# Kernel tuning notes

Measured on AMD Instinct MI355X. Metric: run time of the kernel, lower is better.

The kernel has to match this reference:

```python
import jax, jax.numpy as jnp
import numpy as np

B, N, H = 32, 1024, 128
EPS = 1e-5


def setup_inputs() -> dict:
    key = jax.random.key(0)
    ks = jax.random.split(key, 9)
    node_embeddings = jax.random.normal(ks[0], (B, N, H), dtype=jnp.float32)
    edge_relations = jax.random.normal(ks[1], (B, N, N, 3), dtype=jnp.float32)
    adjacency = jax.random.randint(ks[2], (N, N), 0, 2, dtype=jnp.int32)
    s_msg = 1.0 / np.sqrt(H + 3)
    s_upd = 1.0 / np.sqrt(2 * H)
    W_msg = jax.random.uniform(ks[3], (H, H + 3), jnp.float32, -s_msg, s_msg)
    b_msg = jax.random.uniform(ks[4], (H,), jnp.float32, -s_msg, s_msg)
    W_upd = jax.random.uniform(ks[5], (H, 2 * H), jnp.float32, -s_upd, s_upd)
    b_upd = jax.random.uniform(ks[6], (H,), jnp.float32, -s_upd, s_upd)
    gamma = jnp.ones((H,), jnp.float32)
    beta = jnp.zeros((H,), jnp.float32)
    return {"node_embeddings": node_embeddings, "edge_relations": edge_relations,
            "adjacency": adjacency, "W_msg": W_msg, "b_msg": b_msg,
            "W_upd": W_upd, "b_upd": b_upd, "gamma": gamma, "beta": beta}


def reference(node_embeddings, edge_relations, adjacency, W_msg, b_msg, W_upd, b_upd, gamma, beta):
    # node_embeddings: [B,N,H]; edge_relations: [B,N,N,3]; adjacency: [N,N]
    b_, n_, h_ = node_embeddings.shape
    mask = (adjacency > 0).astype(node_embeddings.dtype)  # mask[j,i]=1 if i is neighbor of j
    # Split msg_nn weight: Linear(cat(h_i, e_ij)) = h_i @ W_h^T + e_ij @ W_e^T + b
    W_h = W_msg[:, :h_]   # [H,H]
    W_e = W_msg[:, h_:]   # [H,3]
    h_part = jnp.einsum('bih,oh->bio', node_embeddings, W_h)       # [B,N,H]
    msg_h = jnp.einsum('ji,bio->bjo', mask, h_part)                # aggregate sender linear part
    e_agg = jnp.einsum('bijc,ji->bjc', edge_relations, mask)       # aggregate edge feats first (memory-bound)
    msg_e = jnp.einsum('bjc,oc->bjo', e_agg, W_e)
    deg = mask.sum(axis=1)                                         # [N] in-degree of j
    messages = msg_h + msg_e + deg[None, :, None] * b_msg          # bias added once per edge
    # Dropout(0.2) is identity in inference; BatchNorm uses batch stats (training-mode math).
    upd_in = jnp.concatenate([node_embeddings, messages], axis=-1)  # [B,N,2H]
    updated = jax.nn.relu(jnp.einsum('bjk,ok->bjo', upd_in, W_upd) + b_upd)
    flat = updated.reshape(-1, h_)
    mean = flat.mean(axis=0)
    var = flat.var(axis=0)  # biased, as BatchNorm1d
    normed = (flat - mean) * jax.lax.rsqrt(var + EPS) * gamma + beta
    return normed.reshape(b_, n_, h_) + node_embeddings
```

## Files before the change

### kernel.cpp

```cpp
#include <hip/hip_runtime.h>
#include <hip/hip_bf16.h>

typedef _Float16 f16;
typedef f16 f16x4 __attribute__((ext_vector_type(4)));
typedef f16 f16x8 __attribute__((ext_vector_type(8)));
typedef float f32x4 __attribute__((ext_vector_type(4)));

#define BB 32
#define NN 1024
#define HH 128
#define ROWS (BB*NN)
#define EPS 1e-5f

__device__ __forceinline__ f16 f2h(float x) { return (f16)x; }

__global__ __launch_bounds__(256) void prep_k(
    const float* __restrict__ node, const int* __restrict__ adj,
    const float* __restrict__ W_msg, const float* __restrict__ W_upd,
    f16* __restrict__ mask_h, float* __restrict__ maskT, float* __restrict__ deg,
    f16* __restrict__ upd_in, f16* __restrict__ Wh, f16* __restrict__ Wupd,
    float* __restrict__ We, float* __restrict__ e_agg, float* __restrict__ sums)
{
  const int blk = blockIdx.x, t = threadIdx.x;
  if (blk < 1024) {
    const int j = blk;
    float d = 0.f;
    for (int i = t; i < NN; i += 256) {
      const int a = (adj[j*NN + i] > 0) ? 1 : 0;
      mask_h[j*NN + i] = a ? (f16)1.0f : (f16)0.0f;
      d += (float)a;
    }
    __shared__ float sh[256];
    sh[t] = d;
    for (int s = 128; s > 0; s >>= 1) {
      __syncthreads();
      if (t < s) sh[t] += sh[t + s];
    }
    __syncthreads();
    if (t == 0) deg[j] = sh[0];
  } else if (blk < 2048) {
    const int bi = (blk - 1024) & 31, bj = (blk - 1024) >> 5;
    __shared__ float tile[32][33];
    const int lx = t & 31, ly0 = t >> 5;
    for (int ly = ly0; ly < 32; ly += 8)
      tile[ly][lx] = (adj[(bj*32 + ly)*NN + bi*32 + lx] > 0) ? 1.0f : 0.0f;
    __syncthreads();
    for (int ly = ly0; ly < 32; ly += 8)
      maskT[(long)(bi*32 + ly)*NN + bj*32 + lx] = tile[lx][ly];
  } else if (blk < 4096) {
    const int base = (blk - 2048) * 512 + t;
    #pragma unroll
    for (int rep = 0; rep < 2; rep++) {
      const int idx = base + rep * 256;
      const float4 v = ((const float4*)node)[idx];
      f16x4 hv; hv[0] = f2h(v.x); hv[1] = f2h(v.y); hv[2] = f2h(v.z); hv[3] = f2h(v.w);
      const int row = idx >> 5;
      const int col = (idx & 31) << 2;
      *(f16x4*)&upd_in[(long)row*256 + col] = hv;
    }
  } else if (blk == 4096) {
    for (int idx = t; idx < HH*HH; idx += 256) {
      const int o = idx >> 7, h = idx & 127;
      Wh[idx] = f2h(W_msg[o*131 + h]);
    }
    for (int idx = t; idx < HH*256; idx += 256) {
      const int o = idx >> 8, k = idx & 255;
      Wupd[idx] = f2h(W_upd[o*256 + k]);
    }
    for (int idx = t; idx < HH*3; idx += 256) {
      const int o = idx / 3, c = idx % 3;
      We[idx] = W_msg[o*131 + 128 + c];
    }
    if (t < 256) sums[t] = 0.f;
  } else {
    const int base = (blk - 4097) * 3072 + t;
    #pragma unroll
    for (int r = 0; r < 12; r++) e_agg[base + r*256] = 0.f;
  }
}

__global__ __launch_bounds__(384) void eagg_k(
    const float* __restrict__ E, const float* __restrict__ maskT,
    float* __restrict__ e_agg)
{
  const int jt = blockIdx.x << 7;
  const int ih = blockIdx.y << 9;
  const int b  = blockIdx.z;
  const int t  = threadIdx.x;
  const int jl = t / 3, c = t % 3;
  const int j  = jt + jl;
  const float* Ep = E + (long)b*3145728 + (long)ih*3072 + jt*3 + t;
  const float* Mp = maskT + (long)ih*NN + j;
  float acc = 0.f;
  for (int i0 = 0; i0 < 512; i0 += 8) {
    float ev[8], mv[8];
    #pragma unroll
    for (int u = 0; u < 8; u++) ev[u] = Ep[(long)(i0 + u)*3072];
    #pragma unroll
    for (int u = 0; u < 8; u++) mv[u] = Mp[(long)(i0 + u)*NN];
    #pragma unroll
    for (int u = 0; u < 8; u++) acc = fmaf(mv[u], ev[u], acc);
  }
  atomicAdd(&e_agg[((long)b*NN + j)*3 + c], acc);
}

template<int MODE>
__global__ __launch_bounds__(256) void gemm_bt_k(
    const f16* __restrict__ Ag, long aBatch, int lda,
    const f16* __restrict__ Bg, long bBatch, int ldb,
    int K, void* __restrict__ outp,
    const float* __restrict__ deg, const float* __restrict__ b_msg,
    const float* __restrict__ e_agg, const float* __restrict__ We,
    const float* __restrict__ b_upd)
{
  const int mt = blockIdx.x, nt = blockIdx.y, bb = blockIdx.z;
  const f16* Ab = Ag + (long)bb*aBatch + (long)mt*128*lda;
  const f16* Bb = Bg + (long)bb*bBatch + (long)nt*128*ldb;
  __shared__ f16 As[128*32];
  __shared__ f16 Bs[128*32];
  const int tid  = threadIdx.x;
  const int lane = tid & 63;
  const int wave = tid >> 6;
  const int wm = (wave & 1) << 6, wn = (wave >> 1) << 6;

  f32x4 acc[4][4];
  #pragma unroll
  for (int i = 0; i < 4; i++)
    #pragma unroll
    for (int j = 0; j < 4; j++)
      #pragma unroll
      for (int r = 0; r < 4; r++) acc[i][j][r] = 0.f;

  for (int k0 = 0; k0 < K; k0 += 32) {
    #pragma unroll
    for (int p = 0; p < 2; p++) {
      const int q = (p << 8) + tid;
      const int row = q >> 2, ks = (q & 3) << 3;
      *(uint4*)&As[(row << 5) + ks] = *(const uint4*)&Ab[(long)row*lda + k0 + ks];
      *(uint4*)&Bs[(row << 5) + ks] = *(const uint4*)&Bb[(long)row*ldb + k0 + ks];
    }
    __syncthreads();
    f16x8 af[4], bf[4];
    #pragma unroll
    for (int i = 0; i < 4; i++) {
      af[i] = *(const f16x8*)&As[((wm + (i << 4) + (lane & 15)) << 5) + ((lane >> 4) << 3)];
      bf[i] = *(const f16x8*)&Bs[((wn + (i << 4) + (lane & 15)) << 5) + ((lane >> 4) << 3)];
    }
    #pragma unroll
    for (int i = 0; i < 4; i++)
      #pragma unroll
      for (int j = 0; j < 4; j++)
        acc[i][j] = __builtin_amdgcn_mfma_f32_16x16x32_f16(af[i], bf[j], acc[i][j], 0, 0, 0);
    __syncthreads();
  }

  const int rb = (lane >> 4) << 2, cb = lane & 15;
  if (MODE == 0) {
    f16* out = (f16*)outp + (long)bb * (HH*NN);
    #pragma unroll
    for (int i = 0; i < 4; i++)
      #pragma unroll
      for (int r = 0; r < 4; r++) {
        const int gm = (mt << 7) + wm + (i << 4) + rb + r;
        #pragma unroll
        for (int j = 0; j < 4; j++) {
          const int gn = (nt << 7) + wn + (j << 4) + cb;
          out[(long)gm*NN + gn] = f2h(acc[i][j][r]);
        }
      }
  } else if (MODE == 1) {
    f16* out = (f16*)outp;
    #pragma unroll
    for (int i = 0; i < 4; i++)
      #pragma unroll
      for (int r = 0; r < 4; r++) {
        const int gm = (mt << 7) + wm + (i << 4) + rb + r;
        const float dg = deg[gm];
        const long eb = ((long)bb*NN + gm)*3;
        const float e0 = e_agg[eb], e1 = e_agg[eb+1], e2 = e_agg[eb+2];
        #pragma unroll
        for (int j = 0; j < 4; j++) {
          const int gn = wn + (j << 4) + cb;
          const float v = acc[i][j][r] + dg*b_msg[gn]
                        + e0*We[gn*3] + e1*We[gn*3+1] + e2*We[gn*3+2];
          out[((long)bb*NN + gm)*256 + 128 + gn] = f2h(v);
        }
      }
  } else {
    float* out = (float*)outp;
    #pragma unroll
    for (int i = 0; i < 4; i++)
      #pragma unroll
      for (int r = 0; r < 4; r++) {
        const int gm = (mt << 7) + wm + (i << 4) + rb + r;
        #pragma unroll
        for (int j = 0; j < 4; j++) {
          const int gn = wn + (j << 4) + cb;
          const float v = acc[i][j][r] + b_upd[gn];
          out[(long)gm*HH + gn] = fmaxf(v, 0.f);
        }
      }
  }
}

__global__ __launch_bounds__(256) void stats_k(const float* __restrict__ upd,
                                               float* __restrict__ sums)
{
  const int t = threadIdx.x, o = t & 127, half = t >> 7;
  const long base = (long)blockIdx.x * 128;
  float s = 0.f, q = 0.f;
  for (int r = half; r < 128; r += 2) {
    const float v = upd[(base + r)*HH + o];
    s += v; q += v*v;
  }
  __shared__ float shs[256], shq[256];
  shs[t] = s; shq[t] = q;
  __syncthreads();
  if (t < 128) {
    atomicAdd(&sums[t],       shs[t] + shs[t + 128]);
    atomicAdd(&sums[128 + t], shq[t] + shq[t + 128]);
  }
}

__global__ __launch_bounds__(256) void final_k(const float* __restrict__ upd,
    const float* __restrict__ node, const float* __restrict__ sums,
    const float* __restrict__ gamma, const float* __restrict__ beta,
    float* __restrict__ out)
{
  const long idx = (long)blockIdx.x*256 + threadIdx.x;
  const float4 u  = ((const float4*)upd)[idx];
  const float4 nd = ((const float4*)node)[idx];
  const int ob = (idx & 31) << 2;
  const float inv = 1.0f/32768.0f;
  float4 res;
  #pragma unroll
  for (int c = 0; c < 4; c++) {
    const float m  = sums[ob + c]*inv;
    const float va = sums[128 + ob + c]*inv - m*m;
    const float sc = rsqrtf(va + EPS)*gamma[ob + c];
    ((float*)&res)[c] = (((const float*)&u)[c] - m)*sc + beta[ob + c]
                      + ((const float*)&nd)[c];
  }
  ((float4*)out)[idx] = res;
}

extern "C" void kernel_launch(void* const* d_in, const int* in_sizes, int n_in,
                              void* d_out, int out_size, void* d_ws, size_t ws_size,
                              hipStream_t stream) {
  const float* node  = (const float*)d_in[0];
  const float* E     = (const float*)d_in[1];
  const int*   adj   = (const int*)  d_in[2];
  const float* W_msg = (const float*)d_in[3];
  const float* b_msg = (const float*)d_in[4];
  const float* W_upd = (const float*)d_in[5];
  const float* b_upd = (const float*)d_in[6];
  const float* gamma = (const float*)d_in[7];
  const float* beta  = (const float*)d_in[8];
  float* out = (float*)d_out;

  char* p = (char*)d_ws;
  auto alloc = [&](size_t n) { void* r = (void*)p; p += (n + 255) & ~(size_t)255; return r; };
  f16*   upd_in   = (f16*)  alloc((size_t)ROWS*256*2);
  f16*   h_part_T = (f16*)  alloc((size_t)BB*HH*NN*2);
  f16*   mask_h   = (f16*)  alloc((size_t)NN*NN*2);
  float* maskT    = (float*)alloc((size_t)NN*NN*4);
  float* updated  = (float*)alloc((size_t)ROWS*HH*4);
  float* e_agg    = (float*)alloc((size_t)BB*NN*3*4);
  f16*   Wh       = (f16*)  alloc((size_t)HH*HH*2);
  f16*   Wupd     = (f16*)  alloc((size_t)HH*256*2);
  float* We       = (float*)alloc((size_t)HH*3*4);
  float* deg      = (float*)alloc((size_t)NN*4);
  float* sums     = (float*)alloc((size_t)256*4);

  prep_k<<<4129, 256, 0, stream>>>(node, adj, W_msg, W_upd, mask_h, maskT, deg,
                                   upd_in, Wh, Wupd, We, e_agg, sums);

  gemm_bt_k<0><<<dim3(1, 8, BB), 256, 0, stream>>>(
      Wh, 0, HH, upd_in, (long)NN*256, 256, HH, h_part_T,
      nullptr, nullptr, nullptr, nullptr, nullptr);

  eagg_k<<<dim3(8, 2, BB), 384, 0, stream>>>(E, maskT, e_agg);

  gemm_bt_k<1><<<dim3(8, 1, BB), 256, 0, stream>>>(
      mask_h, 0, NN, h_part_T, (long)HH*NN, NN, NN, upd_in,
      deg, b_msg, e_agg, We, nullptr);

  gemm_bt_k<2><<<dim3(256, 1, 1), 256, 0, stream>>>(
      upd_in, 0, 256, Wupd, 0, 256, 256, updated,
      nullptr, nullptr, nullptr, nullptr, b_upd);

  stats_k<<<256, 256, 0, stream>>>(updated, sums);
  final_k<<<4096, 256, 0, stream>>>(updated, node, sums, gamma, beta, out);
}
```

Before: 705.2 us.

## Fuse prep, edge aggregation and GEMMs; fold BN stats into update GEMM epilogue

Restructures the pipeline into fewer kernels. The mask transpose and f16 mask buffers are removed, and the mask is built from adjacency on the fly inside the GEMM and the edge aggregation. The h_part GEMM and the edge aggregation now run in one launch as separate block groups, and the f16 conversion of node embeddings is fused into the GEMM loads. BatchNorm column sums are computed in the update GEMM epilogue, and the updated activations are stored as f16. This cuts launches, intermediate traffic and the separate stats pass, at the cost of somewhat lower precision in the stored activations and a less coalesced edge-feature read pattern.

```diff
diff --git a/kernel.cpp b/kernel.cpp
--- a/kernel.cpp
+++ b/kernel.cpp
@@ -14,130 +14,115 @@
 
 __device__ __forceinline__ f16 f2h(float x) { return (f16)x; }
 
-__global__ __launch_bounds__(256) void prep_k(
-    const float* __restrict__ node, const int* __restrict__ adj,
+__global__ __launch_bounds__(256) void prep0_k(
     const float* __restrict__ W_msg, const float* __restrict__ W_upd,
-    f16* __restrict__ mask_h, float* __restrict__ maskT, float* __restrict__ deg,
-    f16* __restrict__ upd_in, f16* __restrict__ Wh, f16* __restrict__ Wupd,
-    float* __restrict__ We, float* __restrict__ e_agg, float* __restrict__ sums)
+    f16* __restrict__ Wh, f16* __restrict__ Wupd, float* __restrict__ We,
+    float* __restrict__ e_agg, float* __restrict__ deg, float* __restrict__ sums)
 {
   const int blk = blockIdx.x, t = threadIdx.x;
-  if (blk < 1024) {
-    const int j = blk;
-    float d = 0.f;
-    for (int i = t; i < NN; i += 256) {
-      const int a = (adj[j*NN + i] > 0) ? 1 : 0;
-      mask_h[j*NN + i] = a ? (f16)1.0f : (f16)0.0f;
-      d += (float)a;
-    }
-    __shared__ float sh[256];
-    sh[t] = d;
-    for (int s = 128; s > 0; s >>= 1) {
-      __syncthreads();
-      if (t < s) sh[t] += sh[t + s];
-    }
-    __syncthreads();
-    if (t == 0) deg[j] = sh[0];
-  } else if (blk < 2048) {
-    const int bi = (blk - 1024) & 31, bj = (blk - 1024) >> 5;
-    __shared__ float tile[32][33];
-    const int lx = t & 31, ly0 = t >> 5;
-    for (int ly = ly0; ly < 32; ly += 8)
-      tile[ly][lx] = (adj[(bj*32 + ly)*NN + bi*32 + lx] > 0) ? 1.0f : 0.0f;
-    __syncthreads();
-    for (int ly = ly0; ly < 32; ly += 8)
-      maskT[(long)(bi*32 + ly)*NN + bj*32 + lx] = tile[lx][ly];
-  } else if (blk < 4096) {
-    const int base = (blk - 2048) * 512 + t;
-    #pragma unroll
-    for (int rep = 0; rep < 2; rep++) {
-      const int idx = base + rep * 256;
-      const float4 v = ((const float4*)node)[idx];
-      f16x4 hv; hv[0] = f2h(v.x); hv[1] = f2h(v.y); hv[2] = f2h(v.z); hv[3] = f2h(v.w);
-      const int row = idx >> 5;
-      const int col = (idx & 31) << 2;
-      *(f16x4*)&upd_in[(long)row*256 + col] = hv;
-    }
-  } else if (blk == 4096) {
+  if (blk == 0) {
     for (int idx = t; idx < HH*HH; idx += 256) {
       const int o = idx >> 7, h = idx & 127;
       Wh[idx] = f2h(W_msg[o*131 + h]);
     }
-    for (int idx = t; idx < HH*256; idx += 256) {
-      const int o = idx >> 8, k = idx & 255;
-      Wupd[idx] = f2h(W_upd[o*256 + k]);
-    }
-    for (int idx = t; idx < HH*3; idx += 256) {
-      const int o = idx / 3, c = idx % 3;
-      We[idx] = W_msg[o*131 + 128 + c];
-    }
+  } else if (blk == 1) {
+    for (int idx = t; idx < HH*256; idx += 256)
+      Wupd[idx] = f2h(W_upd[idx]);
+  } else if (blk == 2) {
+    for (int idx = t; idx < HH*3; idx += 256)
+      We[idx] = W_msg[(idx/3)*131 + 128 + (idx % 3)];
     if (t < 256) sums[t] = 0.f;
+    for (int idx = t; idx < NN; idx += 256) deg[idx] = 0.f;
   } else {
-    const int base = (blk - 4097) * 3072 + t;
-    #pragma unroll
-    for (int r = 0; r < 12; r++) e_agg[base + r*256] = 0.f;
-  }
-}
-
-__global__ __launch_bounds__(384) void eagg_k(
-    const float* __restrict__ E, const float* __restrict__ maskT,
-    float* __restrict__ e_agg)
-{
-  const int jt = blockIdx.x << 7;
-  const int ih = blockIdx.y << 9;
-  const int b  = blockIdx.z;
-  const int t  = threadIdx.x;
-  const int jl = t / 3, c = t % 3;
-  const int j  = jt + jl;
-  const float* Ep = E + (long)b*3145728 + (long)ih*3072 + jt*3 + t;
-  const float* Mp = maskT + (long)ih*NN + j;
-  float acc = 0.f;
-  for (int i0 = 0; i0 < 512; i0 += 8) {
-    float ev[8], mv[8];
-    #pragma unroll
-    for (int u = 0; u < 8; u++) ev[u] = Ep[(long)(i0 + u)*3072];
-    #pragma unroll
-    for (int u = 0; u < 8; u++) mv[u] = Mp[(long)(i0 + u)*NN];
-    #pragma unroll
-    for (int u = 0; u < 8; u++) acc = fmaf(mv[u], ev[u], acc);
-  }
-  atomicAdd(&e_agg[((long)b*NN + j)*3 + c], acc);
-}
-
-template<int MODE>
-__global__ __launch_bounds__(256) void gemm_bt_k(
-    const f16* __restrict__ Ag, long aBatch, int lda,
-    const f16* __restrict__ Bg, long bBatch, int ldb,
-    int K, void* __restrict__ outp,
-    const float* __restrict__ deg, const float* __restrict__ b_msg,
-    const float* __restrict__ e_agg, const float* __restrict__ We,
-    const float* __restrict__ b_upd)
-{
-  const int mt = blockIdx.x, nt = blockIdx.y, bb = blockIdx.z;
-  const f16* Ab = Ag + (long)bb*aBatch + (long)mt*128*lda;
-  const f16* Bb = Bg + (long)bb*bBatch + (long)nt*128*ldb;
+    const int base = (blk - 3) * 24576 + t;
+    #pragma unroll
+    for (int r = 0; r < 96; r++) e_agg[base + r*256] = 0.f;
+  }
+}
+
+__global__ __launch_bounds__(256) void phaseB_k(
+    const float* __restrict__ node, const float* __restrict__ E,
+    const int* __restrict__ adj, const f16* __restrict__ Wh,
+    f16* __restrict__ h_part_T, float* __restrict__ e_agg,
+    float* __restrict__ deg)
+{
   __shared__ f16 As[128*32];
   __shared__ f16 Bs[128*32];
-  const int tid  = threadIdx.x;
-  const int lane = tid & 63;
-  const int wave = tid >> 6;
+  const int tid = threadIdx.x;
+
+  if (blockIdx.x >= 256) {
+    const int e  = blockIdx.x - 256;
+    const int bb = e >> 5;
+    const int r5 = e & 31;
+    const int jt = r5 & 3;
+    const int ih = r5 >> 2;
+    const int j  = (jt << 8) + tid;
+    const int i0 = ih << 7;
+    const float* Ep = E + (long)bb*3145728 + (long)i0*3072 + (long)j*3;
+    const int*   Ap = adj + (long)j*NN + i0;
+    float a0 = 0.f, a1 = 0.f, a2 = 0.f, dc = 0.f;
+    for (int ii = 0; ii < 128; ii += 8) {
+      const int4 m0 = *(const int4*)(Ap + ii);
+      const int4 m1 = *(const int4*)(Ap + ii + 4);
+      float ev[8][3];
+      #pragma unroll
+      for (int v = 0; v < 8; v++) {
+        const float* q = Ep + (long)(ii + v)*3072;
+        ev[v][0] = q[0]; ev[v][1] = q[1]; ev[v][2] = q[2];
+      }
+      const int mm[8] = {m0.x, m0.y, m0.z, m0.w, m1.x, m1.y, m1.z, m1.w};
+      #pragma unroll
+      for (int v = 0; v < 8; v++) {
+        const float m = (mm[v] > 0) ? 1.f : 0.f;
+        a0 = fmaf(m, ev[v][0], a0);
+        a1 = fmaf(m, ev[v][1], a1);
+        a2 = fmaf(m, ev[v][2], a2);
+        dc += m;
+      }
+    }
+    const long eb = ((long)bb*NN + j)*3;
+    atomicAdd(&e_agg[eb],     a0);
+    atomicAdd(&e_agg[eb + 1], a1);
+    atomicAdd(&e_agg[eb + 2], a2);
+    if (bb == 0) atomicAdd(&deg[j], dc);
+    return;
+  }
+
+  const int g  = blockIdx.x;
+  const int nt = g & 7, bb = g >> 3;
+  const int nbase = nt << 7;
+  const int lane = tid & 63, wave = tid >> 6;
   const int wm = (wave & 1) << 6, wn = (wave >> 1) << 6;
 
-  f32x4 acc[4][4];
-  #pragma unroll
-  for (int i = 0; i < 4; i++)
+  f32x4 acc[2][4];
+  #pragma unroll
+  for (int i = 0; i < 2; i++)
     #pragma unroll
     for (int j = 0; j < 4; j++)
       #pragma unroll
       for (int r = 0; r < 4; r++) acc[i][j][r] = 0.f;
-
-  for (int k0 = 0; k0 < K; k0 += 32) {
+  f32x4 acc2[2][4];
+  #pragma unroll
+  for (int i = 0; i < 2; i++)
+    #pragma unroll
+    for (int j = 0; j < 4; j++)
+      #pragma unroll
+      for (int r = 0; r < 4; r++) acc2[i][j][r] = 0.f;
+
+  for (int k0 = 0; k0 < HH; k0 += 32) {
     #pragma unroll
     for (int p = 0; p < 2; p++) {
       const int q = (p << 8) + tid;
       const int row = q >> 2, ks = (q & 3) << 3;
-      *(uint4*)&As[(row << 5) + ks] = *(const uint4*)&Ab[(long)row*lda + k0 + ks];
-      *(uint4*)&Bs[(row << 5) + ks] = *(const uint4*)&Bb[(long)row*ldb + k0 + ks];
+      *(uint4*)&As[(row << 5) + ks] = *(const uint4*)&Wh[(long)row*HH + k0 + ks];
+    }
+    #pragma unroll
+    for (int p = 0; p < 4; p++) {
+      const int q = (p << 8) + tid;
+      const int row = q >> 3, kc = (q & 7) << 2;
+      const float4 v = *(const float4*)&node[(long)((bb << 10) + nbase + row)*HH + k0 + kc];
+      f16x4 hv; hv[0] = f2h(v.x); hv[1] = f2h(v.y); hv[2] = f2h(v.z); hv[3] = f2h(v.w);
+      *(f16x4*)&Bs[(row << 5) + kc] = hv;
     }
     __syncthreads();
     f16x8 af[4], bf[4];
@@ -147,6 +132,80 @@
       bf[i] = *(const f16x8*)&Bs[((wn + (i << 4) + (lane & 15)) << 5) + ((lane >> 4) << 3)];
     }
     #pragma unroll
+    for (int i = 0; i < 2; i++)
+      #pragma unroll
+      for (int j = 0; j < 4; j++) {
+        acc[i][j]  = __builtin_amdgcn_mfma_f32_16x16x32_f16(af[i],     bf[j], acc[i][j],  0, 0, 0);
+        acc2[i][j] = __builtin_amdgcn_mfma_f32_16x16x32_f16(af[i + 2], bf[j], acc2[i][j], 0, 0, 0);
+      }
+    __syncthreads();
+  }
+
+  f16* out = h_part_T + (long)bb * (HH*NN);
+  const int rb = (lane >> 4) << 2, cb = lane & 15;
+  #pragma unroll
+  for (int i = 0; i < 4; i++)
+    #pragma unroll
+    for (int r = 0; r < 4; r++) {
+      const int gm = wm + (i << 4) + rb + r;
+      #pragma unroll
+      for (int j = 0; j < 4; j++) {
+        const int gn = nbase + wn + (j << 4) + cb;
+        const float v = (i < 2) ? acc[i][j][r] : acc2[i - 2][j][r];
+        out[(long)gm*NN + gn] = f2h(v);
+      }
+    }
+}
+
+__global__ __launch_bounds__(256) void gemm1_k(
+    const int* __restrict__ adj, const f16* __restrict__ hp,
+    const float* __restrict__ deg, const float* __restrict__ b_msg,
+    const float* __restrict__ e_agg, const float* __restrict__ We,
+    f16* __restrict__ msgs)
+{
+  const int mt = blockIdx.x, bb = blockIdx.z;
+  const int jb = mt << 7;
+  __shared__ f16 As[128*32];
+  __shared__ f16 Bs[128*32];
+  const int tid = threadIdx.x, lane = tid & 63, wave = tid >> 6;
+  const int wm = (wave & 1) << 6, wn = (wave >> 1) << 6;
+
+  f32x4 acc[4][4];
+  #pragma unroll
+  for (int i = 0; i < 4; i++)
+    #pragma unroll
+    for (int j = 0; j < 4; j++)
+      #pragma unroll
+      for (int r = 0; r < 4; r++) acc[i][j][r] = 0.f;
+
+  for (int k0 = 0; k0 < NN; k0 += 32) {
+    #pragma unroll
+    for (int p = 0; p < 4; p++) {
+      const int q = (p << 8) + tid;
+      const int row = q >> 3, kc = (q & 7) << 2;
+      const int4 m = *(const int4*)&adj[(long)(jb + row)*NN + k0 + kc];
+      f16x4 hv;
+      hv[0] = (m.x > 0) ? (f16)1.0f : (f16)0.0f;
+      hv[1] = (m.y > 0) ? (f16)1.0f : (f16)0.0f;
+      hv[2] = (m.z > 0) ? (f16)1.0f : (f16)0.0f;
+      hv[3] = (m.w > 0) ? (f16)1.0f : (f16)0.0f;
+      *(f16x4*)&As[(row << 5) + kc] = hv;
+    }
+    #pragma unroll
+    for (int p = 0; p < 2; p++) {
+      const int q = (p << 8) + tid;
+      const int row = q >> 2, ks = (q & 3) << 3;
+      *(uint4*)&Bs[(row << 5) + ks] =
+          *(const uint4*)&hp[(long)bb*(HH*NN) + (long)row*NN + k0 + ks];
+    }
+    __syncthreads();
+    f16x8 af[4], bf[4];
+    #pragma unroll
+    for (int i = 0; i < 4; i++) {
+      af[i] = *(const f16x8*)&As[((wm + (i << 4) + (lane & 15)) << 5) + ((lane >> 4) << 3)];
+      bf[i] = *(const f16x8*)&Bs[((wn + (i << 4) + (lane & 15)) << 5) + ((lane >> 4) << 3)];
+    }
+    #pragma unroll
     for (int i = 0; i < 4; i++)
       #pragma unroll
       for (int j = 0; j < 4; j++)
@@ -155,80 +214,123 @@
   }
 
   const int rb = (lane >> 4) << 2, cb = lane & 15;
-  if (MODE == 0) {
-    f16* out = (f16*)outp + (long)bb * (HH*NN);
+  #pragma unroll
+  for (int i = 0; i < 4; i++)
+    #pragma unroll
+    for (int r = 0; r < 4; r++) {
+      const int gm = jb + wm + (i << 4) + rb + r;
+      const float dg = deg[gm];
+      const long eb = ((long)bb*NN + gm)*3;
+      const float e0 = e_agg[eb], e1 = e_agg[eb+1], e2 = e_agg[eb+2];
+      #pragma unroll
+      for (int j = 0; j < 4; j++) {
+        const int gn = wn + (j << 4) + cb;
+        const float v = acc[i][j][r] + dg*b_msg[gn]
+                      + e0*We[gn*3] + e1*We[gn*3+1] + e2*We[gn*3+2];
+        msgs[((long)bb*NN + gm)*HH + gn] = f2h(v);
+      }
+    }
+}
+
+__global__ __launch_bounds__(256) void gemm2_k(
+    const float* __restrict__ node, const f16* __restrict__ msgs,
+    const f16* __restrict__ Wupd, const float* __restrict__ b_upd,
+    f16* __restrict__ upd, float* __restrict__ sums)
+{
+  const int mt = blockIdx.x;
+  const int rowb = mt << 7;
+  __shared__ f16 As[128*32];
+  __shared__ f16 Bs[128*32];
+  __shared__ float colS[128], colQ[128];
+  const int tid = threadIdx.x, lane = tid & 63, wave = tid >> 6;
+  const int wm = (wave & 1) << 6, wn = (wave >> 1) << 6;
+  if (tid < 128) { colS[tid] = 0.f; colQ[tid] = 0.f; }
+
+  f32x4 acc[4][4];
+  #pragma unroll
+  for (int i = 0; i < 4; i++)
+    #pragma unroll
+    for (int j = 0; j < 4; j++)
+      #pragma unroll
+      for (int r = 0; r < 4; r++) acc[i][j][r] = 0.f;
+
+  for (int k0 = 0; k0 < 256; k0 += 32) {
+    if (k0 < HH) {
+      #pragma unroll
+      for (int p = 0; p < 4; p++) {
+        const int q = (p << 8) + tid;
+        const int row = q >> 3, kc = (q & 7) << 2;
+        const float4 v = *(const float4*)&node[(long)(rowb + row)*HH + k0 + kc];
+        f16x4 hv; hv[0] = f2h(v.x); hv[1] = f2h(v.y); hv[2] = f2h(v.z); hv[3] = f2h(v.w);
+        *(f16x4*)&As[(row << 5) + kc] = hv;
+      }
+    } else {
+      #pragma unroll
+      for (int p = 0; p < 2; p++) {
+        const int q = (p << 8) + tid;
+        const int row = q >> 2, ks = (q & 3) << 3;
+        *(uint4*)&As[(row << 5) + ks] =
+            *(const uint4*)&msgs[(long)(rowb + row)*HH + (k0 - HH) + ks];
+      }
+    }
+    #pragma unroll
+    for (int p = 0; p < 2; p++) {
+      const int q = (p << 8) + tid;
+      const int row = q >> 2, ks = (q & 3) << 3;
+      *(uint4*)&Bs[(row << 5) + ks] = *(const uint4*)&Wupd[(long)row*256 + k0 + ks];
+    }
+    __syncthreads();
+    f16x8 af[4], bf[4];
+    #pragma unroll
+    for (int i = 0; i < 4; i++) {
+      af[i] = *(const f16x8*)&As[((wm + (i << 4) + (lane & 15)) << 5) + ((lane >> 4) << 3)];
+      bf[i] = *(const f16x8*)&Bs[((wn + (i << 4) + (lane & 15)) << 5) + ((lane >> 4) << 3)];
+    }
     #pragma unroll
     for (int i = 0; i < 4; i++)
       #pragma unroll
-      for (int r = 0; r < 4; r++) {
-        const int gm = (mt << 7) + wm + (i << 4) + rb + r;
-        #pragma unroll
-        for (int j = 0; j < 4; j++) {
-          const int gn = (nt << 7) + wn + (j << 4) + cb;
-          out[(long)gm*NN + gn] = f2h(acc[i][j][r]);
-        }
-      }
-  } else if (MODE == 1) {
-    f16* out = (f16*)outp;
-    #pragma unroll
-    for (int i = 0; i < 4; i++)
-      #pragma unroll
-      for (int r = 0; r < 4; r++) {
-        const int gm = (mt << 7) + wm + (i << 4) + rb + r;
-        const float dg = deg[gm];
-        const long eb = ((long)bb*NN + gm)*3;
-        const float e0 = e_agg[eb], e1 = e_agg[eb+1], e2 = e_agg[eb+2];
-        #pragma unroll
-        for (int j = 0; j < 4; j++) {
-          const int gn = wn + (j << 4) + cb;
-          const float v = acc[i][j][r] + dg*b_msg[gn]
-                        + e0*We[gn*3] + e1*We[gn*3+1] + e2*We[gn*3+2];
-          out[((long)bb*NN + gm)*256 + 128 + gn] = f2h(v);
-        }
-      }
-  } else {
-    float* out = (float*)outp;
-    #pragma unroll
-    for (int i = 0; i < 4; i++)
-      #pragma unroll
-      for (int r = 0; r < 4; r++) {
-        const int gm = (mt << 7) + wm + (i << 4) + rb + r;
-        #pragma unroll
-        for (int j = 0; j < 4; j++) {
-          const int gn = wn + (j << 4) + cb;
-          const float v = acc[i][j][r] + b_upd[gn];
-          out[(long)gm*HH + gn] = fmaxf(v, 0.f);
-        }
-      }
-  }
-}
-
-__global__ __launch_bounds__(256) void stats_k(const float* __restrict__ upd,
-                                               float* __restrict__ sums)
-{
-  const int t = threadIdx.x, o = t & 127, half = t >> 7;
-  const long base = (long)blockIdx.x * 128;
-  float s = 0.f, q = 0.f;
-  for (int r = half; r < 128; r += 2) {
-    const float v = upd[(base + r)*HH + o];
-    s += v; q += v*v;
-  }
-  __shared__ float shs[256], shq[256];
-  shs[t] = s; shq[t] = q;
+      for (int j = 0; j < 4; j++)
+        acc[i][j] = __builtin_amdgcn_mfma_f32_16x16x32_f16(af[i], bf[j], acc[i][j], 0, 0, 0);
+    __syncthreads();
+  }
+
+  const int rb = (lane >> 4) << 2, cb = lane & 15;
+  float bup[4], s[4] = {0,0,0,0}, qq[4] = {0,0,0,0};
+  #pragma unroll
+  for (int j = 0; j < 4; j++) bup[j] = b_upd[wn + (j << 4) + cb];
+  #pragma unroll
+  for (int i = 0; i < 4; i++)
+    #pragma unroll
+    for (int r = 0; r < 4; r++) {
+      const int gm = rowb + wm + (i << 4) + rb + r;
+      #pragma unroll
+      for (int j = 0; j < 4; j++) {
+        const int gn = wn + (j << 4) + cb;
+        const float v = fmaxf(acc[i][j][r] + bup[j], 0.f);
+        upd[(long)gm*HH + gn] = f2h(v);
+        s[j] += v; qq[j] += v*v;
+      }
+    }
+  #pragma unroll
+  for (int j = 0; j < 4; j++) {
+    const int gn = wn + (j << 4) + cb;
+    atomicAdd(&colS[gn], s[j]);
+    atomicAdd(&colQ[gn], qq[j]);
+  }
   __syncthreads();
-  if (t < 128) {
-    atomicAdd(&sums[t],       shs[t] + shs[t + 128]);
-    atomicAdd(&sums[128 + t], shq[t] + shq[t + 128]);
-  }
-}
-
-__global__ __launch_bounds__(256) void final_k(const float* __restrict__ upd,
+  if (tid < 128) {
+    atomicAdd(&sums[tid],       colS[tid]);
+    atomicAdd(&sums[128 + tid], colQ[tid]);
+  }
+}
+
+__global__ __launch_bounds__(256) void final_k(const f16* __restrict__ upd,
     const float* __restrict__ node, const float* __restrict__ sums,
     const float* __restrict__ gamma, const float* __restrict__ beta,
     float* __restrict__ out)
 {
   const long idx = (long)blockIdx.x*256 + threadIdx.x;
-  const float4 u  = ((const float4*)upd)[idx];
+  const f16x4 u  = *(const f16x4*)&upd[idx << 2];
   const float4 nd = ((const float4*)node)[idx];
   const int ob = (idx & 31) << 2;
   const float inv = 1.0f/32768.0f;
@@ -238,7 +340,7 @@
     const float m  = sums[ob + c]*inv;
     const float va = sums[128 + ob + c]*inv - m*m;
     const float sc = rsqrtf(va + EPS)*gamma[ob + c];
-    ((float*)&res)[c] = (((const float*)&u)[c] - m)*sc + beta[ob + c]
+    ((float*)&res)[c] = ((float)u[c] - m)*sc + beta[ob + c]
                       + ((const float*)&nd)[c];
   }
   ((float4*)out)[idx] = res;
@@ -260,11 +362,9 @@
 
   char* p = (char*)d_ws;
   auto alloc = [&](size_t n) { void* r = (void*)p; p += (n + 255) & ~(size_t)255; return r; };
-  f16*   upd_in   = (f16*)  alloc((size_t)ROWS*256*2);
   f16*   h_part_T = (f16*)  alloc((size_t)BB*HH*NN*2);
-  f16*   mask_h   = (f16*)  alloc((size_t)NN*NN*2);
-  float* maskT    = (float*)alloc((size_t)NN*NN*4);
-  float* updated  = (float*)alloc((size_t)ROWS*HH*4);
+  f16*   msgs     = (f16*)  alloc((size_t)ROWS*HH*2);
+  f16*   upd      = (f16*)  alloc((size_t)ROWS*HH*2);
   float* e_agg    = (float*)alloc((size_t)BB*NN*3*4);
   f16*   Wh       = (f16*)  alloc((size_t)HH*HH*2);
   f16*   Wupd     = (f16*)  alloc((size_t)HH*256*2);
@@ -272,23 +372,13 @@
   float* deg      = (float*)alloc((size_t)NN*4);
   float* sums     = (float*)alloc((size_t)256*4);
 
-  prep_k<<<4129, 256, 0, stream>>>(node, adj, W_msg, W_upd, mask_h, maskT, deg,
-                                   upd_in, Wh, Wupd, We, e_agg, sums);
-
-  gemm_bt_k<0><<<dim3(1, 8, BB), 256, 0, stream>>>(
-      Wh, 0, HH, upd_in, (long)NN*256, 256, HH, h_part_T,
-      nullptr, nullptr, nullptr, nullptr, nullptr);
-
-  eagg_k<<<dim3(8, 2, BB), 384, 0, stream>>>(E, maskT, e_agg);
-
-  gemm_bt_k<1><<<dim3(8, 1, BB), 256, 0, stream>>>(
-      mask_h, 0, NN, h_part_T, (long)HH*NN, NN, NN, upd_in,
-      deg, b_msg, e_agg, We, nullptr);
-
-  gemm_bt_k<2><<<dim3(256, 1, 1), 256, 0, stream>>>(
-      upd_in, 0, 256, Wupd, 0, 256, 256, updated,
-      nullptr, nullptr, nullptr, nullptr, b_upd);
-
-  stats_k<<<256, 256, 0, stream>>>(updated, sums);
-  final_k<<<4096, 256, 0, stream>>>(updated, node, sums, gamma, beta, out);
-}
+  prep0_k<<<7, 256, 0, stream>>>(W_msg, W_upd, Wh, Wupd, We, e_agg, deg, sums);
+
+  phaseB_k<<<1280, 256, 0, stream>>>(node, E, adj, Wh, h_part_T, e_agg, deg);
+
+  gemm1_k<<<dim3(8, 1, BB), 256, 0, stream>>>(adj, h_part_T, deg, b_msg, e_agg, We, msgs);
+
+  gemm2_k<<<256, 256, 0, stream>>>(node, msgs, Wupd, b_upd, upd, sums);
+
+  final_k<<<4096, 256, 0, stream>>>(upd, node, sums, gamma, beta, out);
+}
```

After: 653.6 us. -7.3%, faster.
